# Performance work log

Measured on AMD Instinct MI355X. Metric: run time of the kernel, lower is better.

## Reference

```python
import jax, jax.numpy as jnp
import numpy as np

T = 1000
NUM_CLASSES = 100
BATCH = 256


def setup_inputs() -> dict:
    key = jax.random.key(0)
    k_mu, k_ls, k_eps, k_y = jax.random.split(key, 4)
    mu = jax.random.normal(k_mu, (BATCH, NUM_CLASSES), dtype=jnp.float32)
    log_sigma2 = jax.random.normal(k_ls, (BATCH, NUM_CLASSES), dtype=jnp.float32)
    # MVN(0, I) samples == i.i.d. standard normals; materialized for determinism.
    eps = jax.random.normal(k_eps, (T, BATCH, NUM_CLASSES), dtype=jnp.float32)
    y = jax.random.randint(k_y, (BATCH,), 0, NUM_CLASSES, dtype=jnp.int64)
    return {"mu": mu, "log_sigma2": log_sigma2, "eps": eps, "y": y}


def reference(mu, log_sigma2, eps, y):
    t = eps.shape[0]
    log_T = jnp.asarray(np.log(t), dtype=mu.dtype)
    sigma = jnp.exp(0.5 * log_sigma2)  # [B, C]
    logits = mu[None, :, :] + sigma[None, :, :] * eps  # [T, B, C]
    # per-sample log-probabilities, weighted by 1/T in log-space
    y_hat = jax.nn.log_softmax(logits, axis=-1) - log_T  # [T, B, C]
    log_p = jax.nn.logsumexp(y_hat, axis=0)  # [B, C]
    # nll_loss with mean reduction: -mean over batch of log_p at true class
    picked = jnp.take_along_axis(log_p, y[:, None], axis=1)[:, 0]  # [B]
    return -jnp.mean(picked)
```

## Files before the change

### kernel.cpp

```cpp
#include <hip/hip_runtime.h>

#define T_TOT 1000
#define NCLS  100
#define BATCH 256
#define LOG_T 6.90775527898213705f
#define GRID  2048

__global__ __launch_bounds__(256) void rows_kernel(const float* __restrict__ mu,
                                                   const float* __restrict__ ls2,
                                                   const float* __restrict__ eps,
                                                   const int* __restrict__ y,
                                                   float* __restrict__ partial) {
    const int lane = threadIdx.x & 63;
    const int half = lane >> 5;
    const int j    = lane & 31;
    const int wid  = (blockIdx.x * 256 + threadIdx.x) >> 6;
    const int nw   = (GRID * 256) >> 6;
    const int total_pairs = (T_TOT * BATCH) / 2;

    const int h = 2 * wid + half;
    const int b = h & (BATCH - 1);
    const int yb = y[b];
    const int ks = yb & 3;
    const int owner = yb >> 2;

    float4 m4 = make_float4(0.f, 0.f, 0.f, 0.f);
    float4 s4 = m4;
    if (j < 25) {
        m4 = *(const float4*)(mu  + b * NCLS + 4 * j);
        const float4 l4 = *(const float4*)(ls2 + b * NCLS + 4 * j);
        s4.x = __expf(0.5f * l4.x);
        s4.y = __expf(0.5f * l4.y);
        s4.z = __expf(0.5f * l4.z);
        s4.w = __expf(0.5f * l4.w);
    }

    float acc = 0.f;
    for (int pair = wid; pair < total_pairs; pair += nw) {
        const int r = pair * 2 + half;

        float x0 = -INFINITY, x1 = -INFINITY, x2 = -INFINITY, x3 = -INFINITY;
        if (j < 25) {
            const float4 e4 = *(const float4*)(eps + (size_t)r * NCLS + 4 * j);
            x0 = fmaf(s4.x, e4.x, m4.x);
            x1 = fmaf(s4.y, e4.y, m4.y);
            x2 = fmaf(s4.z, e4.z, m4.z);
            x3 = fmaf(s4.w, e4.w, m4.w);
        }

        float s = __expf(x0) + __expf(x1) + __expf(x2) + __expf(x3);
        #pragma unroll
        for (int off = 1; off <= 16; off <<= 1)
            s += __shfl_xor(s, off, 64);

        if (j == owner) {
            const float px = (ks == 0) ? x0 : (ks == 1) ? x1 : (ks == 2) ? x2 : x3;
            acc += __expf(px - __logf(s));
        }
    }

    if (j == owner) partial[b * 64 + (h >> 8)] = acc;
}

__global__ __launch_bounds__(256) void final_kernel(const float* __restrict__ partial,
                                                    float* __restrict__ out) {
    const int b = threadIdx.x;
    const float4* p4 = (const float4*)(partial + b * 64);
    float s = 0.f;
    #pragma unroll
    for (int i = 0; i < 16; ++i) {
        const float4 a = p4[i];
        s += (a.x + a.y) + (a.z + a.w);
    }
    float lg = __logf(s);

    #pragma unroll
    for (int off = 1; off <= 32; off <<= 1) lg += __shfl_xor(lg, off, 64);

    __shared__ float red[4];
    if ((b & 63) == 0) red[b >> 6] = lg;
    __syncthreads();
    if (b == 0) {
        const float tot = (red[0] + red[1]) + (red[2] + red[3]);
        out[0] = LOG_T - tot * (1.0f / BATCH);
    }
}

extern "C" void kernel_launch(void* const* d_in, const int* in_sizes, int n_in,
                              void* d_out, int out_size, void* d_ws, size_t ws_size,
                              hipStream_t stream) {
    const float* mu  = (const float*)d_in[0];
    const float* ls2 = (const float*)d_in[1];
    const float* eps = (const float*)d_in[2];
    const int*   y   = (const int*)d_in[3];
    float* out     = (float*)d_out;
    float* partial = (float*)d_ws;

    rows_kernel<<<GRID, 256, 0, stream>>>(mu, ls2, eps, y, partial);
    final_kernel<<<1, 256, 0, stream>>>(partial, out);
}
```

Measured before the change: 157.1 us.

## Prefetch next eps row, use DPP reductions, and divide instead of exp-log

The row loop now double-buffers the eps load, fetching the next pair's float4 while computing the current one. The 32-lane sum uses DPP row ops plus a ds_swizzle instead of shfl_xor, which avoids LDS-based shuffles. The per-row probability is computed as exp(x)/S rather than exp(x - log S). The partial buffer is transposed so the final kernel reads coalesced. Masked lanes now start mu at -inf with zero sigma, so the guarded arithmetic drops out of the loop. This relies on the DPP row_shr/ror control encodings forming a correct xor-style reduction within 16-lane rows. Indexing now uses int rather than size_t.

```diff
diff --git a/kernel.cpp b/kernel.cpp
--- a/kernel.cpp
+++ b/kernel.cpp
@@ -5,6 +5,12 @@
 #define BATCH 256
 #define LOG_T 6.90775527898213705f
 #define GRID  2048
+
+template <int CTRL>
+__device__ __forceinline__ float dpp_xor_add(float s) {
+    const int p = __builtin_amdgcn_update_dpp(0, __float_as_int(s), CTRL, 0xF, 0xF, true);
+    return s + __int_as_float(p);
+}
 
 __global__ __launch_bounds__(256) void rows_kernel(const float* __restrict__ mu,
                                                    const float* __restrict__ ls2,
@@ -22,11 +28,12 @@
     const int b = h & (BATCH - 1);
     const int yb = y[b];
     const int ks = yb & 3;
-    const int owner = yb >> 2;
+    const bool isown = (j == (yb >> 2));
 
-    float4 m4 = make_float4(0.f, 0.f, 0.f, 0.f);
-    float4 s4 = m4;
-    if (j < 25) {
+    const bool act = (j < 25);
+    float4 m4 = make_float4(-INFINITY, -INFINITY, -INFINITY, -INFINITY);
+    float4 s4 = make_float4(0.f, 0.f, 0.f, 0.f);
+    if (act) {
         m4 = *(const float4*)(mu  + b * NCLS + 4 * j);
         const float4 l4 = *(const float4*)(ls2 + b * NCLS + 4 * j);
         s4.x = __expf(0.5f * l4.x);
@@ -36,42 +43,46 @@
     }
 
     float acc = 0.f;
-    for (int pair = wid; pair < total_pairs; pair += nw) {
-        const int r = pair * 2 + half;
+    int pair = wid;
+    float4 v = make_float4(0.f, 0.f, 0.f, 0.f);
+    if (act) v = *(const float4*)(eps + (2 * pair + half) * NCLS + 4 * j);
 
-        float x0 = -INFINITY, x1 = -INFINITY, x2 = -INFINITY, x3 = -INFINITY;
-        if (j < 25) {
-            const float4 e4 = *(const float4*)(eps + (size_t)r * NCLS + 4 * j);
-            x0 = fmaf(s4.x, e4.x, m4.x);
-            x1 = fmaf(s4.y, e4.y, m4.y);
-            x2 = fmaf(s4.z, e4.z, m4.z);
-            x3 = fmaf(s4.w, e4.w, m4.w);
-        }
+    while (pair < total_pairs) {
+        const float4 c = v;
+        const int pn = pair + nw;
+        if (act && pn < total_pairs)
+            v = *(const float4*)(eps + (2 * pn + half) * NCLS + 4 * j);
 
-        float s = __expf(x0) + __expf(x1) + __expf(x2) + __expf(x3);
-        #pragma unroll
-        for (int off = 1; off <= 16; off <<= 1)
-            s += __shfl_xor(s, off, 64);
+        const float x0 = fmaf(s4.x, c.x, m4.x);
+        const float x1 = fmaf(s4.y, c.y, m4.y);
+        const float x2 = fmaf(s4.z, c.z, m4.z);
+        const float x3 = fmaf(s4.w, c.w, m4.w);
+        const float e0 = __expf(x0);
+        const float e1 = __expf(x1);
+        const float e2 = __expf(x2);
+        const float e3 = __expf(x3);
+        const float epx = (ks == 0) ? e0 : (ks == 1) ? e1 : (ks == 2) ? e2 : e3;
 
-        if (j == owner) {
-            const float px = (ks == 0) ? x0 : (ks == 1) ? x1 : (ks == 2) ? x2 : x3;
-            acc += __expf(px - __logf(s));
-        }
+        float S = (e0 + e1) + (e2 + e3);
+        S = dpp_xor_add<0xB1>(S);
+        S = dpp_xor_add<0x4E>(S);
+        S = dpp_xor_add<0x141>(S);
+        S = dpp_xor_add<0x140>(S);
+        S += __int_as_float(__builtin_amdgcn_ds_swizzle(__float_as_int(S), 0x401F));
+
+        acc += isown ? __fdividef(epx, S) : 0.f;
+        pair = pn;
     }
 
-    if (j == owner) partial[b * 64 + (h >> 8)] = acc;
+    if (isown) partial[(h >> 8) * BATCH + b] = acc;
 }
 
 __global__ __launch_bounds__(256) void final_kernel(const float* __restrict__ partial,
                                                     float* __restrict__ out) {
     const int b = threadIdx.x;
-    const float4* p4 = (const float4*)(partial + b * 64);
     float s = 0.f;
     #pragma unroll
-    for (int i = 0; i < 16; ++i) {
-        const float4 a = p4[i];
-        s += (a.x + a.y) + (a.z + a.w);
-    }
+    for (int i = 0; i < 64; ++i) s += partial[i * BATCH + b];
     float lg = __logf(s);
 
     #pragma unroll
```

After: 155.5 us. No clear change (-1.0%).
